# Kernel optimization log

Measured on AMD Instinct MI355X. Metric: run time of the kernel, lower is better.

Reference implementation:

```python
import jax, jax.numpy as jnp
import numpy as np

D_MODEL = 1024
D_STATE = 128
D_CONV = 4
EXPAND = 2
HEADDIM = 64
D_INNER = EXPAND * D_MODEL          # 2048
NHEADS = D_INNER // HEADDIM          # 32
CONV_CH = D_INNER + 2 * D_STATE      # conv acts on x, B, C (ngroups=1)
D_IN_PROJ = 2 * D_INNER + 2 * D_STATE + NHEADS
CHUNK = 128


def setup_inputs() -> dict:
    key = jax.random.key(0)
    ks = jax.random.split(key, 8)
    B, L = 4, 2048
    return {
        'x': jax.random.normal(ks[0], (B, L, D_MODEL), jnp.float32),
        'ln_w': jnp.ones((D_MODEL,), jnp.float32),
        'ln_b': jnp.zeros((D_MODEL,), jnp.float32),
        'in_proj_w': jax.random.normal(ks[1], (D_IN_PROJ, D_MODEL), jnp.float32) * 0.02,
        'conv_w': jax.random.normal(ks[2], (CONV_CH, D_CONV), jnp.float32) * 0.2,
        'conv_b': jnp.zeros((CONV_CH,), jnp.float32),
        'dt_bias': jax.random.normal(ks[3], (NHEADS,), jnp.float32) * 0.5,
        'A_log': jax.random.uniform(ks[4], (NHEADS,), jnp.float32, 0.0, 1.5),
        'D': jax.random.normal(ks[5], (NHEADS,), jnp.float32) * 0.1 + 1.0,
        'norm_w': jnp.ones((D_INNER,), jnp.float32),
        'out_proj_w': jax.random.normal(ks[6], (D_MODEL, D_INNER), jnp.float32) * 0.02,
    }


def segsum(a):
    # a: (..., T) -> (..., T, T) with out[i, j] = sum_{j < k <= i} a[k], -inf above diag
    T = a.shape[-1]
    a_rep = jnp.broadcast_to(a[..., :, None], a.shape + (T,))
    a_masked = jnp.where(jnp.tril(jnp.ones((T, T), bool), -1), a_rep, 0.0)
    seg = jnp.cumsum(a_masked, axis=-2)
    return jnp.where(jnp.tril(jnp.ones((T, T), bool), 0), seg, -jnp.inf)


def _ssd(X, a, Bm, Cm):
    # Chunked SSD (Mamba2). X: (b,l,h,p) pre-multiplied by dt; a: (b,l,h)=dt*A; Bm,Cm: (b,l,n)
    b, l, h, p = X.shape
    c = l // CHUNK
    Xc = X.reshape(b, c, CHUNK, h, p)
    Bc = Bm.reshape(b, c, CHUNK, -1)
    Cc = Cm.reshape(b, c, CHUNK, -1)
    ac = a.reshape(b, c, CHUNK, h).transpose(0, 3, 1, 2)   # (b,h,c,q)
    a_cs = jnp.cumsum(ac, axis=-1)                          # (b,h,c,q)
    Lm = jnp.exp(segsum(ac))                                # (b,h,c,q,q)
    # intra-chunk (diagonal) part
    Y_diag = jnp.einsum('bcln,bcsn,bhcls,bcshp->bclhp', Cc, Bc, Lm, Xc)
    # chunk final states
    decay_states = jnp.exp(a_cs[..., -1:] - a_cs)           # (b,h,c,q)
    states = jnp.einsum('bcln,bhcl,bclhp->bchpn', Bc, decay_states, Xc)
    states = jnp.concatenate([jnp.zeros_like(states[:, :1]), states], axis=1)  # (b,c+1,h,p,n)
    a_chunk = jnp.pad(a_cs[..., -1], ((0, 0), (0, 0), (1, 0)))  # (b,h,c+1)
    decay_chunk = jnp.exp(segsum(a_chunk))                  # (b,h,c+1,c+1)
    prev_states = jnp.einsum('bhzc,bchpn->bzhpn', decay_chunk, states)[:, :-1]  # (b,c,h,p,n)
    # inter-chunk (off-diagonal) part
    Y_off = jnp.einsum('bcln,bchpn,bhcl->bclhp', Cc, prev_states, jnp.exp(a_cs))
    return (Y_diag + Y_off).reshape(b, l, h, p)


def reference(x, ln_w, ln_b, in_proj_w, conv_w, conv_b, dt_bias, A_log, D, norm_w, out_proj_w):
    B, L, _ = x.shape
    # pre-LayerNorm
    mu = x.mean(-1, keepdims=True)
    var = ((x - mu) ** 2).mean(-1, keepdims=True)
    h = (x - mu) / jnp.sqrt(var + 1e-5) * ln_w + ln_b
    # Mamba2 in_proj -> [z, xBC, dt]
    zxbcdt = h @ in_proj_w.T
    z = zxbcdt[..., :D_INNER]
    xBC = zxbcdt[..., D_INNER:D_INNER + CONV_CH]
    dt = jax.nn.softplus(zxbcdt[..., -NHEADS:] + dt_bias)  # (B,L,H)
    # causal depthwise conv1d + SiLU
    xp = jnp.pad(xBC, ((0, 0), (D_CONV - 1, 0), (0, 0)))
    conv = sum(xp[:, k:k + L, :] * conv_w[:, k] for k in range(D_CONV)) + conv_b
    xBC = jax.nn.silu(conv)
    xs = xBC[..., :D_INNER].reshape(B, L, NHEADS, HEADDIM)
    Bm = xBC[..., D_INNER:D_INNER + D_STATE]
    Cm = xBC[..., D_INNER + D_STATE:]
    A = -jnp.exp(A_log)                                    # (H,)
    Y = _ssd(xs * dt[..., None], dt * A, Bm, Cm)
    Y = Y + D[None, None, :, None] * xs                    # D skip connection
    y = Y.reshape(B, L, D_INNER)
    # gated RMSNorm (norm_before_gate=False)
    y = y * jax.nn.silu(z)
    y = y * jax.lax.rsqrt(jnp.mean(y * y, -1, keepdims=True) + 1e-5) * norm_w
    out = y @ out_proj_w.T
    # dropout in eval mode = identity; residual
    return out + x
```

## Files before the change

kernel.cpp:

```cpp
#include <hip/hip_runtime.h>
#include <math.h>

#define BATCH   4
#define LSEQ    2048
#define DMODEL  1024
#define DSTATE  128
#define HEADDIM 64
#define DINNER  2048
#define NHEADS  32
#define CONVCH  2304
#define DINPROJ 4384
#define NPAD    4480
#define CHUNKL  128
#define NCHUNK  16
#define ROWS    (BATCH*LSEQ)

#define B_Z     ((size_t)0)
#define B_XBC   (B_Z   + (size_t)ROWS*DINNER*2)
#define B_DT    (B_XBC + (size_t)ROWS*CONVCH*2)
#define B_XS    (B_DT  + (size_t)ROWS*NHEADS*4)
#define B_BC    (B_XS  + (size_t)ROWS*DINNER*2)
#define B_Y     (B_BC  + (size_t)ROWS*256*2)
#define B_ASUM  (B_Y   + (size_t)ROWS*DINNER*2)
#define B_END   (B_ASUM + (size_t)BATCH*NCHUNK*NHEADS*4)

typedef __attribute__((ext_vector_type(8))) short bf16x8;
typedef __attribute__((ext_vector_type(4))) float f32x4;

__device__ __forceinline__ float b2f(ushort u) {
  union { uint32_t i; float f; } v; v.i = ((uint32_t)u) << 16; return v.f;
}
__device__ __forceinline__ ushort f2b(float f) {
  union { float f; uint32_t i; } v; v.f = f;
  uint32_t r = (v.i + 0x7FFFu + ((v.i >> 16) & 1u)) >> 16;
  return (ushort)r;
}

__device__ __forceinline__ void async_ld16(const void* g, void* l) {
  __builtin_amdgcn_global_load_lds(
      (const __attribute__((address_space(1))) unsigned int*)g,
      (__attribute__((address_space(3))) unsigned int*)l, 16, 0, 0);
}


template<int K>
__device__ __forceinline__ void stage_tile(const ushort* __restrict__ A,
    const ushort* __restrict__ W, int m0, int n0, int tid, int t,
    ushort* lA, ushort* lB)
{
  const int k0 = t * 64;
  #pragma unroll
  for (int it = 0; it < 4; it++) {
    int s = it*512 + tid;
    int row = s >> 3;
    int g = (s & 7) ^ (row & 7);
    async_ld16(A + (size_t)(m0 + row)*K + k0 + g*8, lA + (size_t)s*8);
  }
  #pragma unroll
  for (int it = 0; it < 2; it++) {
    int s = it*512 + tid;
    int row = s >> 3;
    int g = (s & 7) ^ (row & 7);
    async_ld16(W + (size_t)(n0 + row)*K + k0 + g*8, lB + (size_t)s*8);
  }
}

__device__ __forceinline__ void compute_tile(const ushort* lA, const ushort* lB,
    int wr, int wc, int rl, int q, f32x4 acc[4][4])
{
  #pragma unroll
  for (int kh = 0; kh < 2; kh++) {
    bf16x8 af[4], bfr[4];
    #pragma unroll
    for (int i = 0; i < 4; i++) {
      int row = wr*64 + i*16 + rl;
      af[i] = *(const bf16x8*)&lA[(size_t)(row*8 + ((kh*4 + q) ^ (row & 7)))*8];
    }
    #pragma unroll
    for (int j = 0; j < 4; j++) {
      int row = wc*64 + j*16 + rl;
      bfr[j] = *(const bf16x8*)&lB[(size_t)(row*8 + ((kh*4 + q) ^ (row & 7)))*8];
    }
    #pragma unroll
    for (int i = 0; i < 4; i++)
      #pragma unroll
      for (int j = 0; j < 4; j++)
        acc[i][j] = __builtin_amdgcn_mfma_f32_16x16x32_bf16(af[i], bfr[j], acc[i][j], 0, 0, 0);
  }
}

__global__ __launch_bounds__(256) void convert_win_kernel(const float* __restrict__ W,
                                                          ushort* __restrict__ Wb)
{
  size_t i = (size_t)blockIdx.x*256 + threadIdx.x;
  Wb[i] = (i < (size_t)DINPROJ*DMODEL) ? f2b(W[i]) : (ushort)0;
}

__global__ __launch_bounds__(256) void convert_wout_kernel(const float* __restrict__ W,
                                                           ushort* __restrict__ Wb)
{
  size_t i = (size_t)blockIdx.x*256 + threadIdx.x;
  Wb[i] = f2b(W[i]);
}

__global__ __launch_bounds__(256) void ln_kernel(const float* __restrict__ x,
    const float* __restrict__ w, const float* __restrict__ bias, ushort* __restrict__ h)
{
  const int row = blockIdx.x;
  const int t = threadIdx.x;
  const float* xr = x + (size_t)row * DMODEL;
  float v[4];
  float s = 0.f;
  #pragma unroll
  for (int i = 0; i < 4; i++) { v[i] = xr[t + i*256]; s += v[i]; }
  __shared__ float red[4];
  #pragma unroll
  for (int o = 32; o > 0; o >>= 1) s += __shfl_down(s, o, 64);
  if ((t & 63) == 0) red[t >> 6] = s;
  __syncthreads();
  float mean = (red[0]+red[1]+red[2]+red[3]) * (1.f/DMODEL);
  float vs = 0.f;
  #pragma unroll
  for (int i = 0; i < 4; i++) { float d = v[i]-mean; vs += d*d; }
  #pragma unroll
  for (int o = 32; o > 0; o >>= 1) vs += __shfl_down(vs, o, 64);
  __syncthreads();
  if ((t & 63) == 0) red[t >> 6] = vs;
  __syncthreads();
  float rstd = rsqrtf((red[0]+red[1]+red[2]+red[3]) * (1.f/DMODEL) + 1e-5f);
  ushort* hr = h + (size_t)row * DMODEL;
  #pragma unroll
  for (int i = 0; i < 4; i++) {
    int c = t + i*256;
    hr[c] = f2b((v[i]-mean)*rstd*w[c] + bias[c]);
  }
}

__global__ __launch_bounds__(512, 2) void gemm_inproj_big(const ushort* __restrict__ A,
    const ushort* __restrict__ W, ushort* __restrict__ z, ushort* __restrict__ xbc,
    float* __restrict__ dtr, const float* __restrict__ dtb)
{
  __shared__ ushort smem[49152];
  ushort* lA0 = smem;
  ushort* lB0 = smem + 32768;
  const int tid = threadIdx.x;
  const int lane = tid & 63;
  const int w = tid >> 6;
  const int wr = w >> 1;
  const int wc = w & 1;
  const int rl = lane & 15;
  const int q  = lane >> 4;

  int orig = blockIdx.y*32 + blockIdx.x;
  int wgid = (orig & 7)*140 + (orig >> 3);
  const int m0 = (wgid & 31) * 256;
  const int n0 = (wgid >> 5) * 128;

  f32x4 acc[4][4];
  #pragma unroll
  for (int i = 0; i < 4; i++)
    #pragma unroll
    for (int j = 0; j < 4; j++) acc[i][j] = (f32x4)(0.f);

  constexpr int NT = DMODEL / 64;
  stage_tile<DMODEL>(A, W, m0, n0, tid, 0, lA0, lB0);
  __syncthreads();
  for (int t = 0; t < NT; t++) {
    ushort* cA = lA0 + (size_t)(t & 1) * 16384;
    ushort* cB = lB0 + (size_t)(t & 1) * 8192;
    if (t + 1 < NT)
      stage_tile<DMODEL>(A, W, m0, n0, tid, t + 1,
                         lA0 + (size_t)((t+1) & 1) * 16384,
                         lB0 + (size_t)((t+1) & 1) * 8192);
    __builtin_amdgcn_s_setprio(1);
    compute_tile(cA, cB, wr, wc, rl, q, acc);
    __builtin_amdgcn_s_setprio(0);
    __syncthreads();
  }

  const int colL = lane & 15;
  const int rowQ = (lane >> 4) * 4;
  if (n0 < DINNER + CONVCH) {
    #pragma unroll
    for (int i = 0; i < 4; i++)
      #pragma unroll
      for (int j = 0; j < 4; j++) {
        int col = wc*64 + j*16 + colL;
        int g = col >> 3;
        #pragma unroll
        for (int r = 0; r < 4; r++) {
          int row = wr*64 + i*16 + rowQ + r;
          smem[row*128 + ((g ^ (row & 7)) << 3) + (col & 7)] = f2b(acc[i][j][r]);
        }
      }
    __syncthreads();
    ushort* outp; int coff, ncols;
    if (n0 < DINNER) { outp = z;   coff = n0;          ncols = DINNER; }
    else             { outp = xbc; coff = n0 - DINNER; ncols = CONVCH; }
    #pragma unroll
    for (int it = 0; it < 8; it++) {
      int idx = tid + it*512;
      int row = idx >> 4, c8 = idx & 15;
      *(uint4*)(outp + (size_t)(m0 + row)*ncols + coff + c8*8) =
          *(const uint4*)&smem[row*128 + ((c8 ^ (row & 7)) << 3)];
    }
  } else {
    if (wc == 0) {
      #pragma unroll
      for (int i = 0; i < 4; i++)
        #pragma unroll
        for (int j = 0; j < 2; j++) {
          int lc = j*16 + colL;
          float bb = dtb[lc];
          #pragma unroll
          for (int r = 0; r < 4; r++) {
            float v = acc[i][j][r] + bb;
            v = (v > 20.f) ? v : log1pf(expf(v));
            dtr[(size_t)(m0 + wr*64 + i*16 + rowQ + r)*NHEADS + lc] = v;
          }
        }
    }
  }
}

__global__ __launch_bounds__(512, 2) void gemm_outproj_big(const ushort* __restrict__ A,
    const ushort* __restrict__ W, const float* __restrict__ x, float* __restrict__ out)
{
  __shared__ ushort smem[49152];
  ushort* lA0 = smem;
  ushort* lB0 = smem + 32768;
  float* fbuf = (float*)smem;
  const int tid = threadIdx.x;
  const int lane = tid & 63;
  const int w = tid >> 6;
  const int wr = w >> 1;
  const int wc = w & 1;
  const int rl = lane & 15;
  const int q  = lane >> 4;

  int orig = blockIdx.y*32 + blockIdx.x;
  int wgid = (orig & 7)*32 + (orig >> 3);
  const int m0 = (wgid & 31) * 256;
  const int n0 = (wgid >> 5) * 128;

  f32x4 acc[4][4];
  #pragma unroll
  for (int i = 0; i < 4; i++)
    #pragma unroll
    for (int j = 0; j < 4; j++) acc[i][j] = (f32x4)(0.f);

  constexpr int NT = DINNER / 64;
  stage_tile<DINNER>(A, W, m0, n0, tid, 0, lA0, lB0);
  __syncthreads();
  for (int t = 0; t < NT; t++) {
    ushort* cA = lA0 + (size_t)(t & 1) * 16384;
    ushort* cB = lB0 + (size_t)(t & 1) * 8192;
    if (t + 1 < NT)
      stage_tile<DINNER>(A, W, m0, n0, tid, t + 1,
                         lA0 + (size_t)((t+1) & 1) * 16384,
                         lB0 + (size_t)((t+1) & 1) * 8192);
    __builtin_amdgcn_s_setprio(1);
    compute_tile(cA, cB, wr, wc, rl, q, acc);
    __builtin_amdgcn_s_setprio(0);
    __syncthreads();
  }

  const int colL = lane & 15;
  const int rowQ = (lane >> 4) * 4;
  #pragma unroll
  for (int h = 0; h < 2; h++) {
    __syncthreads();
    if ((wr >> 1) == h) {
      #pragma unroll
      for (int i = 0; i < 4; i++)
        #pragma unroll
        for (int j = 0; j < 4; j++) {
          int col = wc*64 + j*16 + colL;
          int g = col >> 2;
          #pragma unroll
          for (int r = 0; r < 4; r++) {
            int row = (wr & 1)*64 + i*16 + rowQ + r;
            fbuf[row*128 + ((g ^ (row & 7)) << 2) + (col & 3)] = acc[i][j][r];
          }
        }
    }
    __syncthreads();
    #pragma unroll
    for (int it = 0; it < 8; it++) {
      int idx = tid + it*512;
      int row = idx >> 5, c4 = idx & 31;
      int gm = m0 + h*128 + row;
      float4 xv = *(const float4*)(x + (size_t)gm*DMODEL + n0 + c4*4);
      float4 vv = *(const float4*)&fbuf[row*128 + ((c4 ^ (row & 7)) << 2)];
      vv.x += xv.x; vv.y += xv.y; vv.z += xv.z; vv.w += xv.w;
      *(float4*)(out + (size_t)gm*DMODEL + n0 + c4*4) = vv;
    }
  }
}

__global__ __launch_bounds__(256) void conv_tiled(const ushort* __restrict__ xbc,
    const float* __restrict__ cw, const float* __restrict__ cb,
    ushort* __restrict__ xs, ushort* __restrict__ bcb)
{
  __shared__ ushort tile[35*256];
  const int tid = threadIdx.x;
  const int ch0 = blockIdx.x * 256;
  const int row0 = blockIdx.y * 32;
  const int l0 = row0 & (LSEQ-1);
  for (int idx = tid; idx < 35*32; idx += 256) {
    int r = idx >> 5, c16 = idx & 31;
    uint4 v = make_uint4(0,0,0,0);
    if (l0 + r - 3 >= 0)
      v = *(const uint4*)(xbc + (size_t)(row0 + r - 3)*CONVCH + ch0 + c16*8);
    *(uint4*)&tile[r*256 + c16*8] = v;
  }
  __syncthreads();
  const int ch = ch0 + tid;
  const float w0 = cw[ch*4+0], w1 = cw[ch*4+1], w2 = cw[ch*4+2], w3 = cw[ch*4+3];
  const float bias = cb[ch];
  const bool isX = (ch0 < DINNER);
  #pragma unroll 4
  for (int r = 0; r < 32; r++) {
    float acc = bias;
    acc = fmaf(b2f(tile[(r+0)*256 + tid]), w0, acc);
    acc = fmaf(b2f(tile[(r+1)*256 + tid]), w1, acc);
    acc = fmaf(b2f(tile[(r+2)*256 + tid]), w2, acc);
    acc = fmaf(b2f(tile[(r+3)*256 + tid]), w3, acc);
    float v = acc / (1.f + expf(-acc));
    if (isX) xs[(size_t)(row0 + r)*DINNER + ch] = f2b(v);
    else     bcb[(size_t)(row0 + r)*256 + (ch - DINNER)] = f2b(v);
  }
}

__global__ __launch_bounds__(256) void states_mfma(
    const ushort* __restrict__ xs, const ushort* __restrict__ bcb, const float* __restrict__ dt,
    const float* __restrict__ A_log, ushort* __restrict__ S, float* __restrict__ asum)
{
  constexpr int LDP = 136;
  __shared__ ushort lBT[128*LDP];
  __shared__ ushort lXT[64*LDP];
  __shared__ float dts[CHUNKL], acs[CHUNKL];
  __shared__ float wtot;
  const int hh = blockIdx.x, c = blockIdx.y, b = blockIdx.z;
  const int tid = threadIdx.x;
  const int lane = tid & 63;
  const int w = tid >> 6;
  const int rbase = b*LSEQ + c*CHUNKL;
  const size_t sbase = (size_t)((b*NCHUNK + c)*NHEADS + hh) * 8192;

  float pre = 0.f;
  if (tid < 128) {
    float myv = dt[(size_t)(rbase + tid)*NHEADS + hh];
    dts[tid] = myv;
    pre = myv;
    #pragma unroll
    for (int o = 1; o < 64; o <<= 1) {
      float u = __shfl_up(pre, o, 64);
      if ((tid & 63) >= o) pre += u;
    }
    if (tid == 63) wtot = pre;
  }
  #pragma unroll
  for (int it = 0; it < 8; it++) {
    int chunk = tid + it*256;
    int l = chunk >> 4, n8 = chunk & 15;
    ushort tmp[8];
    *(uint4*)tmp = *(const uint4*)(bcb + (size_t)(rbase + l)*256 + n8*8);
    #pragma unroll
    for (int u = 0; u < 8; u++) lBT[(n8*8+u)*LDP + l] = tmp[u];
  }
  __syncthreads();
  float alast_loc = 0.f;
  if (tid < 128) {
    float Aval = -expf(A_log[hh]);
    float a = (pre + ((tid >= 64) ? wtot : 0.f)) * Aval;
    acs[tid] = a;
    if (tid == 127) { asum[(b*NCHUNK + c)*NHEADS + hh] = a; }
  }
  __syncthreads();
  alast_loc = acs[CHUNKL-1];
  #pragma unroll
  for (int it = 0; it < 4; it++) {
    int chunk = tid + it*256;
    int l = chunk >> 3, p8 = (chunk & 7)*8;
    ushort tmp[8];
    *(uint4*)tmp = *(const uint4*)(xs + (size_t)(rbase + l)*DINNER + hh*HEADDIM + p8);
    float wl = dts[l] * expf(alast_loc - acs[l]);
    #pragma unroll
    for (int u = 0; u < 8; u++) lXT[(p8+u)*LDP + l] = f2b(b2f(tmp[u]) * wl);
  }
  __syncthreads();

  const int rl = lane & 15;
  const int kq = (lane >> 4) * 8;
  const int nb = w * 32;
  f32x4 acc[4][2];
  #pragma unroll
  for (int i = 0; i < 4; i++) { acc[i][0] = (f32x4)(0.f); acc[i][1] = (f32x4)(0.f); }
  #pragma unroll
  for (int k0 = 0; k0 < 128; k0 += 32) {
    bf16x8 af[4], bfr[2];
    #pragma unroll
    for (int i = 0; i < 4; i++) af[i]  = *(const bf16x8*)&lXT[(i*16 + rl)*LDP + k0 + kq];
    #pragma unroll
    for (int j = 0; j < 2; j++) bfr[j] = *(const bf16x8*)&lBT[(nb + j*16 + rl)*LDP + k0 + kq];
    #pragma unroll
    for (int i = 0; i < 4; i++)
      #pragma unroll
      for (int j = 0; j < 2; j++)
        acc[i][j] = __builtin_amdgcn_mfma_f32_16x16x32_bf16(af[i], bfr[j], acc[i][j], 0, 0, 0);
  }
  __syncthreads();
  const int colL = lane & 15;
  const int rowQ = (lane >> 4) * 4;
  #pragma unroll
  for (int i = 0; i < 4; i++)
    #pragma unroll
    for (int j = 0; j < 2; j++)
      #pragma unroll
      for (int r = 0; r < 4; r++)
        lXT[(i*16 + rowQ + r)*LDP + nb + j*16 + colL] = f2b(acc[i][j][r]);
  __syncthreads();
  #pragma unroll
  for (int it = 0; it < 4; it++) {
    int idx = tid + it*256;
    int row = idx >> 4, c8 = idx & 15;
    *(uint4*)(S + sbase + row*128 + c8*8) = *(const uint4*)&lXT[row*LDP + c8*8];
  }
}

__global__ __launch_bounds__(256) void scan_kernel(ushort* __restrict__ S, const float* __restrict__ asum)
{
  const int hh = blockIdx.x, sl = blockIdx.y, b = blockIdx.z;
  const int base0 = sl*2048 + threadIdx.x;
  float carry[8];
  #pragma unroll
  for (int i = 0; i < 8; i++) carry[i] = 0.f;
  for (int c = 0; c < NCHUNK; c++) {
    ushort* Sp = S + (size_t)((b*NCHUNK + c)*NHEADS + hh) * 8192;
    float dec = expf(asum[(b*NCHUNK + c)*NHEADS + hh]);
    #pragma unroll
    for (int i = 0; i < 8; i++) {
      int idx = base0 + i*256;
      float sv = b2f(Sp[idx]);
      Sp[idx] = f2b(carry[i]);
      carry[i] = fmaf(dec, carry[i], sv);
    }
  }
}

__global__ __launch_bounds__(256) void yssd_mfma(
    const ushort* __restrict__ xs, const ushort* __restrict__ bcb, const float* __restrict__ dt,
    const float* __restrict__ A_log, const float* __restrict__ Dvec,
    const ushort* __restrict__ S, ushort* __restrict__ y)
{
  constexpr int LDP = 136;
  __shared__ ushort lM [128*LDP];
  __shared__ ushort lXT[64*LDP];
  __shared__ float dts[CHUNKL], acs[CHUNKL];
  __shared__ float wtot;
  const int hh = blockIdx.x, c = blockIdx.y, b = blockIdx.z;
  const int tid = threadIdx.x;
  const int lane = tid & 63;
  const int w = tid >> 6;
  const int rbase = b*LSEQ + c*CHUNKL;
  const size_t sbase = (size_t)((b*NCHUNK + c)*NHEADS + hh) * 8192;
  const ushort* Bg = bcb + (size_t)rbase*256;
  const ushort* Cg = Bg + 128;

  #pragma unroll
  for (int it = 0; it < 4; it++) {
    int chunk = tid + it*256;
    int s = chunk >> 3, p0 = (chunk & 7)*8;
    ushort tmp[8];
    *(uint4*)tmp = *(const uint4*)(xs + (size_t)(rbase + s)*DINNER + hh*HEADDIM + p0);
    #pragma unroll
    for (int u = 0; u < 8; u++) lXT[(p0+u)*LDP + s] = tmp[u];
  }
  float pre = 0.f;
  if (tid < 128) {
    float myv = dt[(size_t)(rbase + tid)*NHEADS + hh];
    dts[tid] = myv;
    pre = myv;
    #pragma unroll
    for (int o = 1; o < 64; o <<= 1) {
      float u = __shfl_up(pre, o, 64);
      if ((tid & 63) >= o) pre += u;
    }
    if (tid == 63) wtot = pre;
  }
  __syncthreads();
  if (tid < 128) {
    float Aval = -expf(A_log[hh]);
    acs[tid] = (pre + ((tid >= 64) ? wtot : 0.f)) * Aval;
  }

  const int rl = lane & 15;
  const int kq = (lane >> 4) * 8;
  const int colL = lane & 15;
  const int rowQ = (lane >> 4) * 4;

  const int wm = (w & 1) * 64;
  const int wn = (w >> 1) * 64;
  f32x4 G[4][4];
  #pragma unroll
  for (int i = 0; i < 4; i++)
    #pragma unroll
    for (int j = 0; j < 4; j++) G[i][j] = (f32x4)(0.f);
  #pragma unroll
  for (int k0 = 0; k0 < 128; k0 += 32) {
    bf16x8 af[4], bfr[4];
    #pragma unroll
    for (int i = 0; i < 4; i++) af[i]  = *(const bf16x8*)(Cg + (size_t)(wm + i*16 + rl)*256 + k0 + kq);
    #pragma unroll
    for (int j = 0; j < 4; j++) bfr[j] = *(const bf16x8*)(Bg + (size_t)(wn + j*16 + rl)*256 + k0 + kq);
    #pragma unroll
    for (int i = 0; i < 4; i++)
      #pragma unroll
      for (int j = 0; j < 4; j++)
        G[i][j] = __builtin_amdgcn_mfma_f32_16x16x32_bf16(af[i], bfr[j], G[i][j], 0, 0, 0);
  }
  __syncthreads();

  #pragma unroll
  for (int j = 0; j < 4; j++) {
    int sIdx = wn + j*16 + colL;
    float as = acs[sIdx];
    float ds = dts[sIdx];
    #pragma unroll
    for (int i = 0; i < 4; i++) {
      #pragma unroll
      for (int r = 0; r < 4; r++) {
        int lIdx = wm + i*16 + rowQ + r;
        float m = (lIdx >= sIdx) ? G[i][j][r] * expf(acs[lIdx] - as) * ds : 0.f;
        lM[lIdx*LDP + sIdx] = f2b(m);
      }
    }
  }

  const int om = w * 32;
  f32x4 Y[2][4];
  #pragma unroll
  for (int i = 0; i < 2; i++)
    #pragma unroll
    for (int j = 0; j < 4; j++) Y[i][j] = (f32x4)(0.f);
  #pragma unroll
  for (int k0 = 0; k0 < 128; k0 += 32) {
    bf16x8 a2[2], b2[4];
    #pragma unroll
    for (int i = 0; i < 2; i++) a2[i] = *(const bf16x8*)(Cg + (size_t)(om + i*16 + rl)*256 + k0 + kq);
    #pragma unroll
    for (int j = 0; j < 4; j++) b2[j] = *(const bf16x8*)(S + sbase + (size_t)(j*16 + rl)*128 + k0 + kq);
    #pragma unroll
    for (int i = 0; i < 2; i++)
      #pragma unroll
      for (int j = 0; j < 4; j++)
        Y[i][j] = __builtin_amdgcn_mfma_f32_16x16x32_bf16(a2[i], b2[j], Y[i][j], 0, 0, 0);
  }
  #pragma unroll
  for (int i = 0; i < 2; i++)
    #pragma unroll
    for (int r = 0; r < 4; r++) {
      float e = expf(acs[om + i*16 + rowQ + r]);
      #pragma unroll
      for (int j = 0; j < 4; j++) Y[i][j][r] *= e;
    }
  __syncthreads();

  #pragma unroll
  for (int k0 = 0; k0 < 128; k0 += 32) {
    bf16x8 a3[2], b3[4];
    #pragma unroll
    for (int i = 0; i < 2; i++) a3[i] = *(const bf16x8*)&lM[(om + i*16 + rl)*LDP + k0 + kq];
    #pragma unroll
    for (int j = 0; j < 4; j++) b3[j] = *(const bf16x8*)&lXT[(j*16 + rl)*LDP + k0 + kq];
    #pragma unroll
    for (int i = 0; i < 2; i++)
      #pragma unroll
      for (int j = 0; j < 4; j++)
        Y[i][j] = __builtin_amdgcn_mfma_f32_16x16x32_bf16(a3[i], b3[j], Y[i][j], 0, 0, 0);
  }

  const float Dh = Dvec[hh];
  #pragma unroll
  for (int i = 0; i < 2; i++) {
    #pragma unroll
    for (int r = 0; r < 4; r++) {
      int lIdx = om + i*16 + rowQ + r;
      ushort* yrow = y + (size_t)(rbase + lIdx)*DINNER + hh*HEADDIM;
      #pragma unroll
      for (int j = 0; j < 4; j++) {
        int p = j*16 + colL;
        float val = Y[i][j][r] + Dh * b2f(lXT[p*LDP + lIdx]);
        yrow[p] = f2b(val);
      }
    }
  }
}

__global__ __launch_bounds__(256) void rmsnorm_kernel(ushort* __restrict__ y,
    const ushort* __restrict__ z, const float* __restrict__ nw)
{
  const int row = blockIdx.x;
  const int t = threadIdx.x;
  ushort* yr = y + (size_t)row*DINNER;
  const ushort* zr = z + (size_t)row*DINNER;
  float v[8];
  float ss = 0.f;
  #pragma unroll
  for (int i = 0; i < 8; i++) {
    int c = t + i*256;
    float zz = b2f(zr[c]);
    float g = b2f(yr[c]) * (zz / (1.f + expf(-zz)));
    v[i] = g;
    ss += g*g;
  }
  #pragma unroll
  for (int o = 32; o > 0; o >>= 1) ss += __shfl_down(ss, o, 64);
  __shared__ float red[4];
  if ((t & 63) == 0) red[t >> 6] = ss;
  __syncthreads();
  float scale = rsqrtf((red[0]+red[1]+red[2]+red[3]) * (1.f/DINNER) + 1e-5f);
  #pragma unroll
  for (int i = 0; i < 8; i++) {
    int c = t + i*256;
    yr[c] = f2b(v[i]*scale*nw[c]);
  }
}

extern "C" void kernel_launch(void* const* d_in, const int* in_sizes, int n_in,
                              void* d_out, int out_size, void* d_ws, size_t ws_size,
                              hipStream_t stream)
{
  const float* x    = (const float*)d_in[0];
  const float* lnw  = (const float*)d_in[1];
  const float* lnb  = (const float*)d_in[2];
  const float* win  = (const float*)d_in[3];
  const float* cw   = (const float*)d_in[4];
  const float* cb   = (const float*)d_in[5];
  const float* dtb  = (const float*)d_in[6];
  const float* alog = (const float*)d_in[7];
  const float* dvec = (const float*)d_in[8];
  const float* nw   = (const float*)d_in[9];
  const float* wout = (const float*)d_in[10];
  float* out = (float*)d_out;
  char* ws = (char*)d_ws;
  (void)in_sizes; (void)n_in; (void)out_size;

  if (ws_size < B_END) return;

  ushort* zb   = (ushort*)(ws + B_Z);
  ushort* xbcb = (ushort*)(ws + B_XBC);
  float*  dtr  = (float*) (ws + B_DT);
  ushort* xsb  = (ushort*)(ws + B_XS);
  ushort* bcb  = (ushort*)(ws + B_BC);
  ushort* yb   = (ushort*)(ws + B_Y);
  float*  asum = (float*) (ws + B_ASUM);
  ushort* Sb   = xbcb;
  ushort* hb   = yb;
  ushort* winB = (ushort*)(ws + B_Y + (size_t)ROWS*DMODEL*2);
  ushort* woutB= (ushort*)(ws + B_XBC + (size_t)BATCH*NCHUNK*NHEADS*HEADDIM*DSTATE*2);

  hipLaunchKernelGGL(convert_win_kernel, dim3((NPAD*DMODEL)/256), dim3(256), 0, stream, win, winB);
  hipLaunchKernelGGL(ln_kernel, dim3(ROWS), dim3(256), 0, stream, x, lnw, lnb, hb);
  hipLaunchKernelGGL(gemm_inproj_big, dim3(32, 35), dim3(512), 0, stream, hb, winB, zb, xbcb, dtr, dtb);
  hipLaunchKernelGGL(conv_tiled, dim3(9, ROWS/32), dim3(256), 0, stream, xbcb, cw, cb, xsb, bcb);
  hipLaunchKernelGGL(convert_wout_kernel, dim3((DMODEL*DINNER)/256), dim3(256), 0, stream, wout, woutB);
  hipLaunchKernelGGL(states_mfma, dim3(NHEADS, NCHUNK, BATCH), dim3(256), 0, stream,
                     xsb, bcb, dtr, alog, Sb, asum);
  hipLaunchKernelGGL(scan_kernel, dim3(NHEADS, 4, BATCH), dim3(256), 0, stream, Sb, asum);
  hipLaunchKernelGGL(yssd_mfma, dim3(NHEADS, NCHUNK, BATCH), dim3(256), 0, stream,
                     xsb, bcb, dtr, alog, dvec, Sb, yb);
  hipLaunchKernelGGL(rmsnorm_kernel, dim3(ROWS), dim3(256), 0, stream, yb, zb, nw);
  hipLaunchKernelGGL(gemm_outproj_big, dim3(32, 8), dim3(512), 0, stream, yb, woutB, x, out);
}
```

Baseline: 474.7 us.

## Use 256x256 in_proj GEMM tiles with manual vmcnt waits and XCD-aware block mapping

The in_proj GEMM now uses a 256x256 output tile per block (8 waves of 128x64) instead of 256x128. NPAD is raised to 4608 so the N dimension divides into 18 tiles, and the launch becomes a 1D grid of 576 blocks mapped per XCD. Both GEMMs replace __syncthreads with explicit s_waitcnt vmcnt plus s_barrier so the next tile's loads stay in flight across the barrier. Occupancy drops to one block per CU, and the padded N adds some wasted columns of work.

```diff
diff --git a/kernel.cpp b/kernel.cpp
--- a/kernel.cpp
+++ b/kernel.cpp
@@ -10,7 +10,7 @@
 #define NHEADS  32
 #define CONVCH  2304
 #define DINPROJ 4384
-#define NPAD    4480
+#define NPAD    4608
 #define CHUNKL  128
 #define NCHUNK  16
 #define ROWS    (BATCH*LSEQ)
@@ -44,7 +44,7 @@
 
 
 template<int K>
-__device__ __forceinline__ void stage_tile(const ushort* __restrict__ A,
+__device__ __forceinline__ void stage256(const ushort* __restrict__ A,
     const ushort* __restrict__ W, int m0, int n0, int tid, int t,
     ushort* lA, ushort* lB)
 {
@@ -57,6 +57,52 @@
     async_ld16(A + (size_t)(m0 + row)*K + k0 + g*8, lA + (size_t)s*8);
   }
   #pragma unroll
+  for (int it = 0; it < 4; it++) {
+    int s = it*512 + tid;
+    int row = s >> 3;
+    int g = (s & 7) ^ (row & 7);
+    async_ld16(W + (size_t)(n0 + row)*K + k0 + g*8, lB + (size_t)s*8);
+  }
+}
+
+__device__ __forceinline__ void compute256(const ushort* lA, const ushort* lB,
+    int wr, int wc, int rl, int q, f32x4 acc[8][4])
+{
+  #pragma unroll
+  for (int kh = 0; kh < 2; kh++) {
+    bf16x8 af[8], bfr[4];
+    #pragma unroll
+    for (int i = 0; i < 8; i++) {
+      int row = wr*128 + i*16 + rl;
+      af[i] = *(const bf16x8*)&lA[(size_t)(row*8 + ((kh*4 + q) ^ (row & 7)))*8];
+    }
+    #pragma unroll
+    for (int j = 0; j < 4; j++) {
+      int row = wc*64 + j*16 + rl;
+      bfr[j] = *(const bf16x8*)&lB[(size_t)(row*8 + ((kh*4 + q) ^ (row & 7)))*8];
+    }
+    #pragma unroll
+    for (int i = 0; i < 8; i++)
+      #pragma unroll
+      for (int j = 0; j < 4; j++)
+        acc[i][j] = __builtin_amdgcn_mfma_f32_16x16x32_bf16(af[i], bfr[j], acc[i][j], 0, 0, 0);
+  }
+}
+
+template<int K>
+__device__ __forceinline__ void stage_tile(const ushort* __restrict__ A,
+    const ushort* __restrict__ W, int m0, int n0, int tid, int t,
+    ushort* lA, ushort* lB)
+{
+  const int k0 = t * 64;
+  #pragma unroll
+  for (int it = 0; it < 4; it++) {
+    int s = it*512 + tid;
+    int row = s >> 3;
+    int g = (s & 7) ^ (row & 7);
+    async_ld16(A + (size_t)(m0 + row)*K + k0 + g*8, lA + (size_t)s*8);
+  }
+  #pragma unroll
   for (int it = 0; it < 2; it++) {
     int s = it*512 + tid;
     int row = s >> 3;
@@ -136,61 +182,66 @@
   }
 }
 
-__global__ __launch_bounds__(512, 2) void gemm_inproj_big(const ushort* __restrict__ A,
+__global__ __launch_bounds__(512, 1) void gemm_inproj_256(const ushort* __restrict__ A,
     const ushort* __restrict__ W, ushort* __restrict__ z, ushort* __restrict__ xbc,
     float* __restrict__ dtr, const float* __restrict__ dtb)
 {
-  __shared__ ushort smem[49152];
-  ushort* lA0 = smem;
-  ushort* lB0 = smem + 32768;
+  __shared__ ushort smem[65536];
   const int tid = threadIdx.x;
   const int lane = tid & 63;
   const int w = tid >> 6;
-  const int wr = w >> 1;
-  const int wc = w & 1;
+  const int wr = w >> 2;
+  const int wc = w & 3;
   const int rl = lane & 15;
   const int q  = lane >> 4;
 
-  int orig = blockIdx.y*32 + blockIdx.x;
-  int wgid = (orig & 7)*140 + (orig >> 3);
-  const int m0 = (wgid & 31) * 256;
-  const int n0 = (wgid >> 5) * 128;
-
-  f32x4 acc[4][4];
-  #pragma unroll
-  for (int i = 0; i < 4; i++)
+  const int orig = blockIdx.x;
+  const int xcd  = orig & 7;
+  const int jj   = orig >> 3;
+  const int m0 = (xcd*4 + jj/18) * 256;
+  const int n0 = (jj % 18) * 256;
+
+  f32x4 acc[8][4];
+  #pragma unroll
+  for (int i = 0; i < 8; i++)
     #pragma unroll
     for (int j = 0; j < 4; j++) acc[i][j] = (f32x4)(0.f);
 
   constexpr int NT = DMODEL / 64;
-  stage_tile<DMODEL>(A, W, m0, n0, tid, 0, lA0, lB0);
-  __syncthreads();
+  stage256<DMODEL>(A, W, m0, n0, tid, 0, smem, smem + 16384);
   for (int t = 0; t < NT; t++) {
-    ushort* cA = lA0 + (size_t)(t & 1) * 16384;
-    ushort* cB = lB0 + (size_t)(t & 1) * 8192;
-    if (t + 1 < NT)
-      stage_tile<DMODEL>(A, W, m0, n0, tid, t + 1,
-                         lA0 + (size_t)((t+1) & 1) * 16384,
-                         lB0 + (size_t)((t+1) & 1) * 8192);
+    const ushort* cA = smem + (t & 1)*32768;
+    const ushort* cB = cA + 16384;
+    if (t + 1 < NT) {
+      ushort* nA = smem + ((t+1) & 1)*32768;
+      stage256<DMODEL>(A, W, m0, n0, tid, t + 1, nA, nA + 16384);
+      asm volatile("s_waitcnt vmcnt(8)" ::: "memory");
+    } else {
+      asm volatile("s_waitcnt vmcnt(0)" ::: "memory");
+    }
+    __builtin_amdgcn_s_barrier();
+    __builtin_amdgcn_sched_barrier(0);
     __builtin_amdgcn_s_setprio(1);
-    compute_tile(cA, cB, wr, wc, rl, q, acc);
+    compute256(cA, cB, wr, wc, rl, q, acc);
     __builtin_amdgcn_s_setprio(0);
-    __syncthreads();
+    __builtin_amdgcn_sched_barrier(0);
+    __builtin_amdgcn_s_barrier();
   }
 
   const int colL = lane & 15;
   const int rowQ = (lane >> 4) * 4;
   if (n0 < DINNER + CONVCH) {
     #pragma unroll
-    for (int i = 0; i < 4; i++)
+    for (int i = 0; i < 8; i++)
       #pragma unroll
       for (int j = 0; j < 4; j++) {
         int col = wc*64 + j*16 + colL;
         int g = col >> 3;
         #pragma unroll
         for (int r = 0; r < 4; r++) {
-          int row = wr*64 + i*16 + rowQ + r;
-          smem[row*128 + ((g ^ (row & 7)) << 3) + (col & 7)] = f2b(acc[i][j][r]);
+          int row = wr*128 + i*16 + rowQ + r;
+          int p = (g & 24) | ((g ^ row) & 7);
+          smem[row*256 + p*8 + (col & 7)] = f2b(acc[i][j][r]);
         }
       }
     __syncthreads();
@@ -198,16 +249,17 @@
     if (n0 < DINNER) { outp = z;   coff = n0;          ncols = DINNER; }
     else             { outp = xbc; coff = n0 - DINNER; ncols = CONVCH; }
     #pragma unroll
-    for (int it = 0; it < 8; it++) {
+    for (int it = 0; it < 16; it++) {
       int idx = tid + it*512;
-      int row = idx >> 4, c8 = idx & 15;
-      *(uint4*)(outp + (size_t)(m0 + row)*ncols + coff + c8*8) =
-          *(const uint4*)&smem[row*128 + ((c8 ^ (row & 7)) << 3)];
+      int row = idx >> 5, g = idx & 31;
+      int p = (g & 24) | ((g ^ row) & 7);
+      *(uint4*)(outp + (size_t)(m0 + row)*ncols + coff + g*8) =
+          *(const uint4*)&smem[row*256 + p*8];
     }
   } else {
     if (wc == 0) {
       #pragma unroll
-      for (int i = 0; i < 4; i++)
+      for (int i = 0; i < 8; i++)
         #pragma unroll
         for (int j = 0; j < 2; j++) {
           int lc = j*16 + colL;
@@ -216,14 +268,14 @@
           for (int r = 0; r < 4; r++) {
             float v = acc[i][j][r] + bb;
             v = (v > 20.f) ? v : log1pf(expf(v));
-            dtr[(size_t)(m0 + wr*64 + i*16 + rowQ + r)*NHEADS + lc] = v;
+            dtr[(size_t)(m0 + wr*128 + i*16 + rowQ + r)*NHEADS + lc] = v;
           }
         }
     }
   }
 }
 
-__global__ __launch_bounds__(512, 2) void gemm_outproj_big(const ushort* __restrict__ A,
+__global__ __launch_bounds__(512, 1) void gemm_outproj_big(const ushort* __restrict__ A,
     const ushort* __restrict__ W, const float* __restrict__ x, float* __restrict__ out)
 {
   __shared__ ushort smem[49152];
@@ -238,10 +290,11 @@
   const int rl = lane & 15;
   const int q  = lane >> 4;
 
-  int orig = blockIdx.y*32 + blockIdx.x;
-  int wgid = (orig & 7)*32 + (orig >> 3);
-  const int m0 = (wgid & 31) * 256;
-  const int n0 = (wgid >> 5) * 128;
+  const int orig = blockIdx.x;
+  const int xcd  = orig & 7;
+  const int jj   = orig >> 3;
+  const int m0 = (xcd*4 + (jj >> 3)) * 256;
+  const int n0 = (jj & 7) * 128;
 
   f32x4 acc[4][4];
   #pragma unroll
@@ -251,18 +304,24 @@
 
   constexpr int NT = DINNER / 64;
   stage_tile<DINNER>(A, W, m0, n0, tid, 0, lA0, lB0);
-  __syncthreads();
   for (int t = 0; t < NT; t++) {
-    ushort* cA = lA0 + (size_t)(t & 1) * 16384;
-    ushort* cB = lB0 + (size_t)(t & 1) * 8192;
-    if (t + 1 < NT)
+    const ushort* cA = lA0 + (size_t)(t & 1) * 16384;
+    const ushort* cB = lB0 + (size_t)(t & 1) * 8192;
+    if (t + 1 < NT) {
       stage_tile<DINNER>(A, W, m0, n0, tid, t + 1,
                          lA0 + (size_t)((t+1) & 1) * 16384,
                          lB0 + (size_t)((t+1) & 1) * 8192);
+      asm volatile("s_waitcnt vmcnt(6)" ::: "memory");
+    } else {
+      asm volatile("s_waitcnt vmcnt(0)" ::: "memory");
+    }
+    __builtin_amdgcn_s_barrier();
+    __builtin_amdgcn_sched_barrier(0);
     __builtin_amdgcn_s_setprio(1);
     compute_tile(cA, cB, wr, wc, rl, q, acc);
     __builtin_amdgcn_s_setprio(0);
-    __syncthreads();
+    __builtin_amdgcn_sched_barrier(0);
+    __builtin_amdgcn_s_barrier();
   }
 
   const int colL = lane & 15;
@@ -663,7 +722,7 @@
 
   hipLaunchKernelGGL(convert_win_kernel, dim3((NPAD*DMODEL)/256), dim3(256), 0, stream, win, winB);
   hipLaunchKernelGGL(ln_kernel, dim3(ROWS), dim3(256), 0, stream, x, lnw, lnb, hb);
-  hipLaunchKernelGGL(gemm_inproj_big, dim3(32, 35), dim3(512), 0, stream, hb, winB, zb, xbcb, dtr, dtb);
+  hipLaunchKernelGGL(gemm_inproj_256, dim3(576), dim3(512), 0, stream, hb, winB, zb, xbcb, dtr, dtb);
   hipLaunchKernelGGL(conv_tiled, dim3(9, ROWS/32), dim3(256), 0, stream, xbcb, cw, cb, xsb, bcb);
   hipLaunchKernelGGL(convert_wout_kernel, dim3((DMODEL*DINNER)/256), dim3(256), 0, stream, wout, woutB);
   hipLaunchKernelGGL(states_mfma, dim3(NHEADS, NCHUNK, BATCH), dim3(256), 0, stream,
@@ -672,5 +731,5 @@
   hipLaunchKernelGGL(yssd_mfma, dim3(NHEADS, NCHUNK, BATCH), dim3(256), 0, stream,
                      xsb, bcb, dtr, alog, dvec, Sb, yb);
   hipLaunchKernelGGL(rmsnorm_kernel, dim3(ROWS), dim3(256), 0, stream, yb, zb, nw);
-  hipLaunchKernelGGL(gemm_outproj_big, dim3(32, 8), dim3(512), 0, stream, yb, woutB, x, out);
-}
+  hipLaunchKernelGGL(gemm_outproj_big, dim3(256), dim3(512), 0, stream, yb, woutB, x, out);
+}
```

Measured after the change: 473.3 us. Within noise of the previous version (-0.3%).

## Remap GEMM block scheduling per XCD and shrink out-proj tiles to 128x128

Applied to the files above, without the earlier changes.

The in-projection GEMM now uses a 1D grid whose block-to-tile mapping groups M-tiles by XCD, and its launch bounds drop to one block per CU. The out-projection GEMM is replaced by a 256-thread, 128x128-tile kernel with single-buffered LDS staging (gemm_core_swz) and 512 blocks instead of 256. The goal is better L2 locality across XCDs and more blocks to fill the device, at the cost of losing double-buffered prefetch in the out-projection. NPAD is also raised to 4608 so the padded weight conversion covers 36 column tiles.

```diff
diff --git a/kernel.cpp b/kernel.cpp
--- a/kernel.cpp
+++ b/kernel.cpp
@@ -10,7 +10,7 @@
 #define NHEADS  32
 #define CONVCH  2304
 #define DINPROJ 4384
-#define NPAD    4480
+#define NPAD    4608
 #define CHUNKL  128
 #define NCHUNK  16
 #define ROWS    (BATCH*LSEQ)
@@ -42,7 +42,6 @@
       (__attribute__((address_space(3))) unsigned int*)l, 16, 0, 0);
 }
 
-
 template<int K>
 __device__ __forceinline__ void stage_tile(const ushort* __restrict__ A,
     const ushort* __restrict__ W, int m0, int n0, int tid, int t,
@@ -89,6 +88,50 @@
   }
 }
 
+template<int K>
+__device__ __forceinline__ void gemm_core_swz(const ushort* __restrict__ A,
+    const ushort* __restrict__ W, int m0, int n0, int tid,
+    ushort* lA, ushort* lB, f32x4 acc[4][4])
+{
+  const int lane = tid & 63;
+  const int w = tid >> 6;
+  const int wm = (w & 1) * 64;
+  const int wn = (w >> 1) * 64;
+  const int rl = lane & 15;
+  const int q  = lane >> 4;
+  for (int k0 = 0; k0 < K; k0 += 64) {
+    __syncthreads();
+    #pragma unroll
+    for (int is = 0; is < 4; is++) {
+      int s = (w*4 + is)*64 + lane;
+      int row = s >> 3;
+      int g = (s & 7) ^ (row & 7);
+      async_ld16(A + (size_t)(m0 + row)*K + k0 + g*8, lA + (size_t)s*8);
+      async_ld16(W + (size_t)(n0 + row)*K + k0 + g*8, lB + (size_t)s*8);
+    }
+    __syncthreads();
+    #pragma unroll
+    for (int kh = 0; kh < 2; kh++) {
+      bf16x8 af[4], bfr[4];
+      #pragma unroll
+      for (int i = 0; i < 4; i++) {
+        int row = wm + i*16 + rl;
+        af[i] = *(const bf16x8*)&lA[(size_t)(row*8 + ((kh*4 + q) ^ (row & 7)))*8];
+      }
+      #pragma unroll
+      for (int j = 0; j < 4; j++) {
+        int row = wn + j*16 + rl;
+        bfr[j] = *(const bf16x8*)&lB[(size_t)(row*8 + ((kh*4 + q) ^ (row & 7)))*8];
+      }
+      #pragma unroll
+      for (int i = 0; i < 4; i++)
+        #pragma unroll
+        for (int j = 0; j < 4; j++)
+          acc[i][j] = __builtin_amdgcn_mfma_f32_16x16x32_bf16(af[i], bfr[j], acc[i][j], 0, 0, 0);
+    }
+  }
+}
+
 __global__ __launch_bounds__(256) void convert_win_kernel(const float* __restrict__ W,
                                                           ushort* __restrict__ Wb)
 {
@@ -136,7 +179,7 @@
   }
 }
 
-__global__ __launch_bounds__(512, 2) void gemm_inproj_big(const ushort* __restrict__ A,
+__global__ __launch_bounds__(512, 1) void gemm_inproj_v6(const ushort* __restrict__ A,
     const ushort* __restrict__ W, ushort* __restrict__ z, ushort* __restrict__ xbc,
     float* __restrict__ dtr, const float* __restrict__ dtb)
 {
@@ -151,10 +194,11 @@
   const int rl = lane & 15;
   const int q  = lane >> 4;
 
-  int orig = blockIdx.y*32 + blockIdx.x;
-  int wgid = (orig & 7)*140 + (orig >> 3);
-  const int m0 = (wgid & 31) * 256;
-  const int n0 = (wgid >> 5) * 128;
+  const int orig = blockIdx.x;
+  const int xcd  = orig & 7;
+  const int jj   = orig >> 3;
+  const int m0 = (xcd*4 + jj/35) * 256;
+  const int n0 = (jj % 35) * 128;
 
   f32x4 acc[4][4];
   #pragma unroll
@@ -223,63 +267,47 @@
   }
 }
 
-__global__ __launch_bounds__(512, 2) void gemm_outproj_big(const ushort* __restrict__ A,
+__global__ __launch_bounds__(256) void gemm_outproj_mfma(const ushort* __restrict__ A,
     const ushort* __restrict__ W, const float* __restrict__ x, float* __restrict__ out)
 {
-  __shared__ ushort smem[49152];
-  ushort* lA0 = smem;
-  ushort* lB0 = smem + 32768;
+  __shared__ ushort smem[16384];
+  ushort* lA = smem;
+  ushort* lB = smem + 8192;
   float* fbuf = (float*)smem;
   const int tid = threadIdx.x;
   const int lane = tid & 63;
   const int w = tid >> 6;
-  const int wr = w >> 1;
-  const int wc = w & 1;
-  const int rl = lane & 15;
-  const int q  = lane >> 4;
-
-  int orig = blockIdx.y*32 + blockIdx.x;
-  int wgid = (orig & 7)*32 + (orig >> 3);
-  const int m0 = (wgid & 31) * 256;
-  const int n0 = (wgid >> 5) * 128;
-
+
+  const int orig = blockIdx.x;
+  const int xcd  = orig & 7;
+  const int jj   = orig >> 3;
+  const int m0 = (xcd*8 + (jj >> 3)) * 128;
+  const int n0 = (jj & 7) * 128;
+
+  const int wn = (w >> 1) * 64;
   f32x4 acc[4][4];
   #pragma unroll
   for (int i = 0; i < 4; i++)
     #pragma unroll
     for (int j = 0; j < 4; j++) acc[i][j] = (f32x4)(0.f);
 
-  constexpr int NT = DINNER / 64;
-  stage_tile<DINNER>(A, W, m0, n0, tid, 0, lA0, lB0);
-  __syncthreads();
-  for (int t = 0; t < NT; t++) {
-    ushort* cA = lA0 + (size_t)(t & 1) * 16384;
-    ushort* cB = lB0 + (size_t)(t & 1) * 8192;
-    if (t + 1 < NT)
-      stage_tile<DINNER>(A, W, m0, n0, tid, t + 1,
-                         lA0 + (size_t)((t+1) & 1) * 16384,
-                         lB0 + (size_t)((t+1) & 1) * 8192);
-    __builtin_amdgcn_s_setprio(1);
-    compute_tile(cA, cB, wr, wc, rl, q, acc);
-    __builtin_amdgcn_s_setprio(0);
-    __syncthreads();
-  }
+  gemm_core_swz<DINNER>(A, W, m0, n0, tid, lA, lB, acc);
 
   const int colL = lane & 15;
   const int rowQ = (lane >> 4) * 4;
   #pragma unroll
-  for (int h = 0; h < 2; h++) {
+  for (int h0 = 0; h0 < 2; h0++) {
     __syncthreads();
-    if ((wr >> 1) == h) {
+    if ((w & 1) == h0) {
       #pragma unroll
       for (int i = 0; i < 4; i++)
         #pragma unroll
         for (int j = 0; j < 4; j++) {
-          int col = wc*64 + j*16 + colL;
+          int col = wn + j*16 + colL;
           int g = col >> 2;
           #pragma unroll
           for (int r = 0; r < 4; r++) {
-            int row = (wr & 1)*64 + i*16 + rowQ + r;
+            int row = i*16 + rowQ + r;
             fbuf[row*128 + ((g ^ (row & 7)) << 2) + (col & 3)] = acc[i][j][r];
           }
         }
@@ -287,9 +315,9 @@
     __syncthreads();
     #pragma unroll
     for (int it = 0; it < 8; it++) {
-      int idx = tid + it*512;
+      int idx = tid + it*256;
       int row = idx >> 5, c4 = idx & 31;
-      int gm = m0 + h*128 + row;
+      int gm = m0 + h0*64 + row;
       float4 xv = *(const float4*)(x + (size_t)gm*DMODEL + n0 + c4*4);
       float4 vv = *(const float4*)&fbuf[row*128 + ((c4 ^ (row & 7)) << 2)];
       vv.x += xv.x; vv.y += xv.y; vv.z += xv.z; vv.w += xv.w;
@@ -663,7 +691,7 @@
 
   hipLaunchKernelGGL(convert_win_kernel, dim3((NPAD*DMODEL)/256), dim3(256), 0, stream, win, winB);
   hipLaunchKernelGGL(ln_kernel, dim3(ROWS), dim3(256), 0, stream, x, lnw, lnb, hb);
-  hipLaunchKernelGGL(gemm_inproj_big, dim3(32, 35), dim3(512), 0, stream, hb, winB, zb, xbcb, dtr, dtb);
+  hipLaunchKernelGGL(gemm_inproj_v6, dim3(1120), dim3(512), 0, stream, hb, winB, zb, xbcb, dtr, dtb);
   hipLaunchKernelGGL(conv_tiled, dim3(9, ROWS/32), dim3(256), 0, stream, xbcb, cw, cb, xsb, bcb);
   hipLaunchKernelGGL(convert_wout_kernel, dim3((DMODEL*DINNER)/256), dim3(256), 0, stream, wout, woutB);
   hipLaunchKernelGGL(states_mfma, dim3(NHEADS, NCHUNK, BATCH), dim3(256), 0, stream,
@@ -672,5 +700,5 @@
   hipLaunchKernelGGL(yssd_mfma, dim3(NHEADS, NCHUNK, BATCH), dim3(256), 0, stream,
                      xsb, bcb, dtr, alog, dvec, Sb, yb);
   hipLaunchKernelGGL(rmsnorm_kernel, dim3(ROWS), dim3(256), 0, stream, yb, zb, nw);
-  hipLaunchKernelGGL(gemm_outproj_big, dim3(32, 8), dim3(512), 0, stream, yb, woutB, x, out);
-}
+  hipLaunchKernelGGL(gemm_outproj_mfma, dim3(512), dim3(256), 0, stream, yb, woutB, x, out);
+}
```

After: 461.4 us. 1.03x faster.
